# Optimization experiments

Hardware: AMD Instinct MI355X
Metric: run time of the kernel (lower is better)

Reference implementation:

```python
import jax, jax.numpy as jnp
import numpy as np

B, N, HID = 4, 1024, 256
NH, DH = 8, 32          # heads, head dim (HID = NH*DH)
BH = 64                 # bias MLP hidden


def setup_inputs() -> dict:
    key = jax.random.key(0)
    ks = jax.random.split(key, 12)
    s = lambda fan_in: 1.0 / np.sqrt(fan_in)
    return {
        "h": jax.random.normal(ks[0], (B, N, HID), jnp.float32),
        "coord": jax.random.uniform(ks[1], (B, N), jnp.float32),
        "mask": jnp.ones((B, N), jnp.int32),
        # qkv / proj linear params (stored [in, out])
        "Wqkv": jax.random.normal(ks[2], (HID, 3 * HID), jnp.float32) * s(HID),
        "bqkv": jnp.zeros((3 * HID,), jnp.float32),
        "Wproj": jax.random.normal(ks[3], (HID, HID), jnp.float32) * s(HID),
        "bproj": jnp.zeros((HID,), jnp.float32),
        # layernorm
        "gamma": jnp.ones((HID,), jnp.float32),
        "beta": jnp.zeros((HID,), jnp.float32),
        # relative-bias MLP: Linear(1->BH), SiLU, Linear(BH->BH), SiLU, Linear(BH->NH)
        "Wb1": jax.random.normal(ks[4], (1, BH), jnp.float32),
        "bb1": jnp.zeros((BH,), jnp.float32),
        "Wb2": jax.random.normal(ks[5], (BH, BH), jnp.float32) * s(BH),
        "bb2": jnp.zeros((BH,), jnp.float32),
        "Wb3": jax.random.normal(ks[6], (BH, NH), jnp.float32) * s(BH),
        "bb3": jnp.zeros((NH,), jnp.float32),
    }


def _layernorm(x, gamma, beta, eps=1e-5):
    mu = jnp.mean(x, axis=-1, keepdims=True)
    var = jnp.mean((x - mu) ** 2, axis=-1, keepdims=True)
    return (x - mu) * jax.lax.rsqrt(var + eps) * gamma + beta


def reference(h, coord, mask, Wqkv, bqkv, Wproj, bproj, gamma, beta,
              Wb1, bb1, Wb2, bb2, Wb3, bb3):
    x = _layernorm(h, gamma, beta)                      # [B,N,HID]
    qkv = x @ Wqkv + bqkv                               # [B,N,3*HID]
    q, k, v = jnp.split(qkv, 3, axis=-1)
    # [B,N,HID] -> [B,NH,N,DH]
    reshape = lambda t: t.reshape(B, N, NH, DH).transpose(0, 2, 1, 3)
    q, k, v = reshape(q), reshape(k), reshape(v)

    attn = jnp.einsum("bhqd,bhkd->bhqk", q, k) / np.sqrt(DH).astype(np.float32)

    # pairwise coordinate differences and learned bias
    dcoord = coord[:, None, :] - coord[:, :, None]      # [B,N,N]
    t = dcoord[..., None]                               # [B,N,N,1]
    t = jax.nn.silu(t @ Wb1 + bb1)                      # [B,N,N,BH]
    t = jax.nn.silu(t @ Wb2 + bb2)                      # [B,N,N,BH]
    bias = (t @ Wb3 + bb3)                              # [B,N,N,NH]
    attn = attn + bias.transpose(0, 3, 1, 2)            # [B,NH,N,N]

    neg_inf = jnp.array(-jnp.inf, attn.dtype)
    attn = jnp.where(mask[:, None, None, :] == 0, neg_inf, attn)
    w = jax.nn.softmax(attn, axis=-1)

    out = jnp.einsum("bhqk,bhkd->bhqd", w, v)           # [B,NH,N,DH]
    out = out.transpose(0, 2, 1, 3).reshape(B, N, HID)
    out = out @ Wproj + bproj
    return h + out
```

## Files before the change

kernel.cpp:

```cpp
#include <hip/hip_runtime.h>
#include <hip/hip_fp16.h>
#include <math.h>

#define BB   4
#define NN   1024
#define HIDD 256
#define NHD  8
#define DHD  32
#define BHD  64
#define TI4  4096
#define TBS  4104
#define NSPL 2
#define LOG2E 1.4426950408889634f

typedef __attribute__((ext_vector_type(8))) short bf16x8;
typedef __attribute__((ext_vector_type(4))) short bf16x4;
typedef __attribute__((ext_vector_type(4))) float f32x4;

__device__ __forceinline__ unsigned short f2bf(float x) {
  union { float f; unsigned u; } c; c.f = x;
  unsigned r = c.u + 0x7FFFu + ((c.u >> 16) & 1u);
  return (unsigned short)(r >> 16);
}
__device__ __forceinline__ float bf2f(unsigned short b) {
  union { unsigned u; float f; } c; c.u = ((unsigned)b) << 16;
  return c.f;
}

__device__ __forceinline__ void pv_mfma(f32x4& acc, bf16x4 a, bf16x4 b) {
#if __has_builtin(__builtin_amdgcn_mfma_f32_16x16x16bf16_1k)
  acc = __builtin_amdgcn_mfma_f32_16x16x16bf16_1k(a, b, acc, 0, 0, 0);
#else
  asm volatile("s_nop 1\n\t"
               "v_mfma_f32_16x16x16_bf16 %0, %1, %2, %0\n\t"
               "s_nop 7\n\t"
               "s_nop 3"
               : "+v"(acc) : "v"(a), "v"(b));
#endif
}

__global__ __launch_bounds__(256) void prep_kernel(
    const float* __restrict__ Wb1, const float* __restrict__ bb1,
    const float* __restrict__ Wb2, const float* __restrict__ bb2,
    const float* __restrict__ Wb3, const float* __restrict__ bb3,
    const float* __restrict__ Wqkv, const float* __restrict__ Wproj,
    unsigned short* __restrict__ tblb, unsigned short* __restrict__ wtq,
    unsigned short* __restrict__ wtp)
{
  __shared__ float h1a[4][64], h2a[4][64];
  __shared__ float t[16][17];
  int bid = blockIdx.x, tid = threadIdx.x;
  if (bid < 1025) {
    int g = tid >> 6, j = tid & 63;
    int pt = bid * 4 + g;
    float tt = -1.0f + (float)pt * (2.0f / (float)TI4);
    float z0 = fmaf(tt, Wb1[j], bb1[j]);
    h1a[g][j] = z0 / (1.0f + __expf(-z0));
    __syncthreads();
    float a0 = bb2[j];
    #pragma unroll 16
    for (int i = 0; i < BHD; ++i) a0 = fmaf(h1a[g][i], Wb2[i*BHD + j], a0);
    h2a[g][j] = a0 / (1.0f + __expf(-a0));
    __syncthreads();
    if (j < NHD && pt <= TI4) {
      float o0 = bb3[j];
      #pragma unroll 16
      for (int i = 0; i < BHD; ++i) o0 = fmaf(h2a[g][i], Wb3[i*NHD + j], o0);
      tblb[j*TBS + pt] = f2bf(o0 * LOG2E);
    }
  } else {
    const float* W; unsigned short* Wt; int n0, k0, ncols;
    if (bid < 1793) {
      int rb = bid - 1025;
      n0 = (rb % 48) * 16; k0 = (rb / 48) * 16; ncols = 768;
      W = Wqkv; Wt = wtq;
    } else {
      int rc = bid - 1793;
      n0 = (rc & 15) * 16; k0 = (rc >> 4) * 16; ncols = 256;
      W = Wproj; Wt = wtp;
    }
    int sx = tid & 15, sy = tid >> 4;
    t[sy][sx] = W[(size_t)(k0 + sy) * ncols + n0 + sx];
    __syncthreads();
    Wt[(size_t)(n0 + sy) * 256 + k0 + sx] = f2bf(t[sx][sy]);
  }
}

__global__ __launch_bounds__(256) void ln_qkv_mm_kernel(
    const float* __restrict__ h, const float* __restrict__ gamma,
    const float* __restrict__ beta, const unsigned short* __restrict__ Wt,
    const float* __restrict__ bqkv,
    unsigned short* __restrict__ qws, unsigned short* __restrict__ kws,
    unsigned short* __restrict__ vtws)
{
  __shared__ unsigned short xs[16][260];
  int tid = threadIdx.x;
  int m0 = blockIdx.x * 16, n0 = blockIdx.y * 128;

  {
    int r = tid >> 4, q = tid & 15;
    const float* hrow = h + (size_t)(m0 + r)*HIDD + q*16;
    float4 xv[4];
    float sum = 0.f, sq = 0.f;
    #pragma unroll
    for (int j = 0; j < 4; ++j) {
      xv[j] = *(const float4*)&hrow[j*4];
      sum += xv[j].x + xv[j].y + xv[j].z + xv[j].w;
      sq  += xv[j].x*xv[j].x + xv[j].y*xv[j].y + xv[j].z*xv[j].z + xv[j].w*xv[j].w;
    }
    sum += __shfl_xor(sum, 1); sq += __shfl_xor(sq, 1);
    sum += __shfl_xor(sum, 2); sq += __shfl_xor(sq, 2);
    sum += __shfl_xor(sum, 4); sq += __shfl_xor(sq, 4);
    sum += __shfl_xor(sum, 8); sq += __shfl_xor(sq, 8);
    float mu  = sum * (1.0f/HIDD);
    float var = sq  * (1.0f/HIDD) - mu*mu;
    float rs  = rsqrtf(var + 1e-5f);
    #pragma unroll
    for (int j2 = 0; j2 < 2; ++j2) {
      union { bf16x8 v; unsigned short u[8]; } o;
      #pragma unroll
      for (int e = 0; e < 2; ++e) {
        float4 x4 = xv[j2*2 + e];
        int col = q*16 + j2*8 + e*4;
        float4 gv = *(const float4*)&gamma[col];
        float4 bv = *(const float4*)&beta[col];
        o.u[e*4+0] = f2bf(fmaf((x4.x - mu)*rs, gv.x, bv.x));
        o.u[e*4+1] = f2bf(fmaf((x4.y - mu)*rs, gv.y, bv.y));
        o.u[e*4+2] = f2bf(fmaf((x4.z - mu)*rs, gv.z, bv.z));
        o.u[e*4+3] = f2bf(fmaf((x4.w - mu)*rs, gv.w, bv.w));
      }
      *(bf16x8*)&xs[r][q*16 + j2*8] = o.v;
    }
  }
  __syncthreads();

  int lane = tid & 63, w = tid >> 6;
  int lo = lane & 15, hi = lane >> 4;
  int cw = w * 32;
  f32x4 acc[2];
  acc[0] = (f32x4){0.f,0.f,0.f,0.f};
  acc[1] = (f32x4){0.f,0.f,0.f,0.f};

  #pragma unroll
  for (int ks = 0; ks < 8; ++ks) {
    bf16x8 af = *(const bf16x8*)&xs[lo][ks*32 + hi*8];
    #pragma unroll
    for (int nt = 0; nt < 2; ++nt) {
      bf16x8 bf = *(const bf16x8*)&Wt[(size_t)(n0 + cw + nt*16 + lo)*256 + ks*32 + hi*8];
      acc[nt] = __builtin_amdgcn_mfma_f32_16x16x32_bf16(af, bf, acc[nt], 0, 0, 0);
    }
  }

  int b = m0 >> 10;
  if (n0 < 512) {
    unsigned short* dst = (n0 < 256) ? qws : kws;
    int nbase = (m0 & 1023) + hi*4;
    #pragma unroll
    for (int nt = 0; nt < 2; ++nt) {
      int c = n0 + cw + nt*16 + lo;
      int cr = c & 255;
      int head = cr >> 5, d = cr & 31;
      float bq = bqkv[c];
      size_t bh = (size_t)(b*NHD + head);
      #pragma unroll
      for (int r = 0; r < 4; ++r)
        dst[(bh*NN + nbase + r)*DHD + d] = f2bf(acc[nt][r] + bq);
    }
  } else {
    __syncthreads();
    unsigned short (*vt)[20] = (unsigned short(*)[20])&xs[0][0];
    #pragma unroll
    for (int nt = 0; nt < 2; ++nt) {
      int cr = cw + nt*16 + lo;
      float bq = bqkv[n0 + cr];
      union { unsigned short u[4]; unsigned wd[2]; } pk;
      #pragma unroll
      for (int r = 0; r < 4; ++r) pk.u[r] = f2bf(acc[nt][r] + bq);
      int col = hi*4;
      *(unsigned*)&vt[cr][col]     = pk.wd[0];
      *(unsigned*)&vt[cr][col + 2] = pk.wd[1];
    }
    __syncthreads();
    int nn0 = m0 & 1023;
    int row = tid >> 1, ch = tid & 1;
    int cr256 = (n0 - 512) + row;
    int head = cr256 >> 5, d = cr256 & 31;
    *(bf16x8*)&vtws[((size_t)(b*NHD + head)*DHD + d)*NN + nn0 + ch*8] =
        *(const bf16x8*)&vt[row][ch*8];
  }
}

__global__ __launch_bounds__(256, 4) void attn_kernel(
    const unsigned short* __restrict__ Q, const unsigned short* __restrict__ K,
    const unsigned short* __restrict__ Vt, const float* __restrict__ coord,
    const int* __restrict__ mask, const unsigned short* __restrict__ tblb,
    unsigned short* __restrict__ pO, float2* __restrict__ pML)
{
  __shared__ unsigned short tableL[TBS];
  __shared__ unsigned short Klds[2][64][40];
  __shared__ unsigned short Vtlds[2][32][72];
  __shared__ __align__(16) float ckL[NN/NSPL];
  __shared__ __align__(16) int   mkL[NN/NSPL];

  int tid = threadIdx.x, lane = tid & 63, w = tid >> 6;
  int bh = blockIdx.y, half = blockIdx.z;
  int b = bh >> 3, head = bh & 7;
  int qbase = blockIdx.x * 64 + w * 16;
  int lo = lane & 15, hi = lane >> 4;

  {
    const uint4* src = (const uint4*)(tblb + head*TBS);
    uint4* dst = (uint4*)tableL;
    for (int i = tid; i < TBS/8; i += 256) dst[i] = src[i];
  }

  bf16x8 qf = *(const bf16x8*)&Q[((size_t)bh*NN + qbase + lo)*DHD + hi*8];
  float qoff2 = fmaf(coord[b*NN + qbase + lo], -(float)TI4*0.5f, (float)TI4*0.5f);

  float m = -1e30f, l = 0.f;
  f32x4 oacc[2];
  oacc[0] = (f32x4){0.f,0.f,0.f,0.f};
  oacc[1] = (f32x4){0.f,0.f,0.f,0.f};
  const float scale2 = 0.17677669529663689f * LOG2E;

  int kt0 = half * (NN/NSPL);
  int sr = tid >> 2, ss = tid & 3;
  int vr = tid >> 3, vs = tid & 7;
  {
    #pragma unroll
    for (int i = 0; i < (NN/NSPL)/256; ++i) {
      int idx = i*256 + tid;
      ckL[idx] = coord[b*NN + kt0 + idx];
      mkL[idx] = mask [b*NN + kt0 + idx];
    }
    *(bf16x8*)&Klds[0][sr][ss*8] =
        *(const bf16x8*)&K[((size_t)bh*NN + kt0 + sr)*DHD + ss*8];
    *(bf16x8*)&Vtlds[0][vr][vs*8] =
        *(const bf16x8*)&Vt[((size_t)bh*DHD + vr)*NN + kt0 + vs*8];
  }
  __syncthreads();

  for (int t = 0; t < NN/NSPL/64; ++t) {
    int kt = kt0 + t*64;
    int cur = t & 1;
    bf16x8 kn, vn;
    if (t < NN/NSPL/64 - 1) {
      kn = *(const bf16x8*)&K[((size_t)bh*NN + kt + 64 + sr)*DHD + ss*8];
      vn = *(const bf16x8*)&Vt[((size_t)bh*DHD + vr)*NN + kt + 64 + vs*8];
    }
    float ck[4][4]; int mk[4][4];
    #pragma unroll
    for (int nt = 0; nt < 4; ++nt) {
      float4 c4 = *(const float4*)&ckL[t*64 + nt*16 + hi*4];
      int4   m4 = *(const int4*)  &mkL[t*64 + nt*16 + hi*4];
      ck[nt][0] = c4.x; ck[nt][1] = c4.y; ck[nt][2] = c4.z; ck[nt][3] = c4.w;
      mk[nt][0] = m4.x; mk[nt][1] = m4.y; mk[nt][2] = m4.z; mk[nt][3] = m4.w;
    }

    f32x4 z = {0.f,0.f,0.f,0.f};
    f32x4 sacc[4];
    #pragma unroll
    for (int nt = 0; nt < 4; ++nt) {
      bf16x8 kf = *(const bf16x8*)&Klds[cur][nt*16 + lo][hi*8];
      sacc[nt] = __builtin_amdgcn_mfma_f32_16x16x32_bf16(kf, qf, z, 0, 0, 0);
    }

    float sv[4][4];
    #pragma unroll
    for (int nt = 0; nt < 4; ++nt) {
      #pragma unroll
      for (int r = 0; r < 4; ++r) {
        float u = fmaf(ck[nt][r], (float)TI4*0.5f, qoff2);
        int i0 = (int)(u + 0.5f);
        float bias = bf2f(tableL[i0]);
        float s = fmaf(sacc[nt][r], scale2, bias);
        sv[nt][r] = mk[nt][r] ? s : -1e31f;
      }
    }

    float pm = sv[0][0];
    #pragma unroll
    for (int nt = 0; nt < 4; ++nt)
      #pragma unroll
      for (int r = 0; r < 4; ++r) pm = fmaxf(pm, sv[nt][r]);
    pm = fmaxf(pm, __shfl_xor(pm, 16));
    pm = fmaxf(pm, __shfl_xor(pm, 32));
    float mn = fmaxf(m, pm);
    if (mn > m) {
      float sf = __builtin_amdgcn_exp2f(m - mn);
      l *= sf;
      #pragma unroll
      for (int n2 = 0; n2 < 2; ++n2)
        #pragma unroll
        for (int r = 0; r < 4; ++r) oacc[n2][r] *= sf;
      m = mn;
    }

    bf16x4 pfrag[4];
    #pragma unroll
    for (int nt = 0; nt < 4; ++nt) {
      float p0 = __builtin_amdgcn_exp2f(sv[nt][0] - m);
      float p1 = __builtin_amdgcn_exp2f(sv[nt][1] - m);
      float p2 = __builtin_amdgcn_exp2f(sv[nt][2] - m);
      float p3 = __builtin_amdgcn_exp2f(sv[nt][3] - m);
      l += (p0 + p1) + (p2 + p3);
      union { bf16x4 v; unsigned short u[4]; } pk;
      pk.u[0] = f2bf(p0); pk.u[1] = f2bf(p1);
      pk.u[2] = f2bf(p2); pk.u[3] = f2bf(p3);
      pfrag[nt] = pk.v;
    }

    #pragma unroll
    for (int nt = 0; nt < 4; ++nt) {
      #pragma unroll
      for (int n2 = 0; n2 < 2; ++n2) {
        bf16x4 vf = *(const bf16x4*)&Vtlds[cur][n2*16 + lo][nt*16 + hi*4];
        pv_mfma(oacc[n2], vf, pfrag[nt]);
      }
    }

    if (t < NN/NSPL/64 - 1) {
      *(bf16x8*)&Klds[cur^1][sr][ss*8] = kn;
      *(bf16x8*)&Vtlds[cur^1][vr][vs*8] = vn;
    }
    __syncthreads();
  }

  l += __shfl_xor(l, 16);
  l += __shfl_xor(l, 32);
  size_t base = ((size_t)(half*BB*NHD + bh)*NN + qbase + lo);
  #pragma unroll
  for (int n2 = 0; n2 < 2; ++n2) {
    union { bf16x4 v; unsigned short u[4]; } ov;
    ov.u[0] = f2bf(oacc[n2][0]); ov.u[1] = f2bf(oacc[n2][1]);
    ov.u[2] = f2bf(oacc[n2][2]); ov.u[3] = f2bf(oacc[n2][3]);
    *(bf16x4*)&pO[base*DHD + n2*16 + hi*4] = ov.v;
  }
  if (hi == 0) pML[base] = make_float2(m, l);
}

__global__ __launch_bounds__(256) void combine_kernel(
    const unsigned short* __restrict__ pO, const float2* __restrict__ pML,
    unsigned short* __restrict__ aob)
{
  int idx = blockIdx.x * 256 + threadIdx.x;
  int rg = idx >> 2, d8 = (idx & 3) << 3;
  int bh = rg >> 10, n = rg & 1023;
  int b = bh >> 3, head = bh & 7;
  float2 ml0 = pML[rg];
  float2 ml1 = pML[(size_t)(BB*NHD)*NN + rg];
  float mm = fmaxf(ml0.x, ml1.x);
  float e0 = __builtin_amdgcn_exp2f(ml0.x - mm);
  float e1 = __builtin_amdgcn_exp2f(ml1.x - mm);
  float inv = 1.0f / fmaf(ml0.y, e0, ml1.y * e1);
  e0 *= inv; e1 *= inv;
  union { bf16x8 v; unsigned short u[8]; } a, c, o;
  a.v = *(const bf16x8*)&pO[(size_t)rg*DHD + d8];
  c.v = *(const bf16x8*)&pO[((size_t)(BB*NHD)*NN + rg)*DHD + d8];
  #pragma unroll
  for (int e = 0; e < 8; ++e)
    o.u[e] = f2bf(fmaf(bf2f(a.u[e]), e0, bf2f(c.u[e]) * e1));
  *(bf16x8*)&aob[((size_t)(b*NN + n))*HIDD + head*DHD + d8] = o.v;
}

__global__ __launch_bounds__(256) void proj_mm_kernel(
    const unsigned short* __restrict__ AO, const unsigned short* __restrict__ Wpt,
    const float* __restrict__ bp, const float* __restrict__ h,
    float* __restrict__ out)
{
  int tid = threadIdx.x, lane = tid & 63, w = tid >> 6;
  int lo = lane & 15, hi = lane >> 4;
  int m0 = blockIdx.x * 32 + (w & 1) * 16;
  int n0 = blockIdx.y * 32 + (w >> 1) * 16;
  f32x4 acc = (f32x4){0.f,0.f,0.f,0.f};

  #pragma unroll
  for (int ks = 0; ks < 8; ++ks) {
    bf16x8 af = *(const bf16x8*)&AO[(size_t)(m0 + lo)*256 + ks*32 + hi*8];
    bf16x8 bf = *(const bf16x8*)&Wpt[(size_t)(n0 + lo)*256 + ks*32 + hi*8];
    acc = __builtin_amdgcn_mfma_f32_16x16x32_bf16(af, bf, acc, 0, 0, 0);
  }

  int c = n0 + lo;
  float bpv = bp[c];
  #pragma unroll
  for (int r = 0; r < 4; ++r) {
    size_t o = (size_t)(m0 + hi*4 + r)*HIDD + c;
    out[o] = h[o] + acc[r] + bpv;
  }
}

extern "C" void kernel_launch(void* const* d_in, const int* in_sizes, int n_in,
                              void* d_out, int out_size, void* d_ws, size_t ws_size,
                              hipStream_t stream)
{
  const float* h     = (const float*)d_in[0];
  const float* coord = (const float*)d_in[1];
  const int*   mask  = (const int*)  d_in[2];
  const float* Wqkv  = (const float*)d_in[3];
  const float* bqkv  = (const float*)d_in[4];
  const float* Wproj = (const float*)d_in[5];
  const float* bproj = (const float*)d_in[6];
  const float* gamma = (const float*)d_in[7];
  const float* beta  = (const float*)d_in[8];
  const float* Wb1   = (const float*)d_in[9];
  const float* bb1   = (const float*)d_in[10];
  const float* Wb2   = (const float*)d_in[11];
  const float* bb2   = (const float*)d_in[12];
  const float* Wb3   = (const float*)d_in[13];
  const float* bb3   = (const float*)d_in[14];
  float* out = (float*)d_out;

  unsigned short* tblb = (unsigned short*)d_ws;
  float2* pML = (float2*)(tblb + NHD*TBS);
  unsigned short* wtq  = (unsigned short*)(pML + (size_t)NSPL*BB*NHD*NN);
  unsigned short* wtp  = wtq + 768*256;
  unsigned short* qws  = wtp + 256*256;
  unsigned short* kws  = qws + (size_t)BB*NHD*NN*DHD;
  unsigned short* vtws = kws + (size_t)BB*NHD*NN*DHD;
  unsigned short* pO   = vtws + (size_t)BB*NHD*NN*DHD;
  unsigned short* aob  = pO + (size_t)NSPL*BB*NHD*NN*DHD;

  prep_kernel<<<dim3(2049), dim3(256), 0, stream>>>(
      Wb1, bb1, Wb2, bb2, Wb3, bb3, Wqkv, Wproj, tblb, wtq, wtp);
  ln_qkv_mm_kernel<<<dim3(BB*NN/16, 6), dim3(256), 0, stream>>>(
      h, gamma, beta, wtq, bqkv, qws, kws, vtws);
  attn_kernel<<<dim3(NN/64, BB*NHD, NSPL), dim3(256), 0, stream>>>(
      qws, kws, vtws, coord, mask, tblb, pO, pML);
  combine_kernel<<<dim3(512), dim3(256), 0, stream>>>(pO, pML, aob);
  proj_mm_kernel<<<dim3(BB*NN/32, HIDD/32), dim3(256), 0, stream>>>(
      aob, wtp, bproj, h, out);
}
```

Baseline: 65.73 us.

## Fuse split-combine into projection GEMM and use lazy softmax rescaling

Removes the separate combine kernel. The projection kernel now merges the two split-KV partial outputs into shared memory before its MFMA loop, which saves one launch and the aob round trip through global memory. The cost is redundant work: each of the 8 column blocks recomputes the same combine for its 32 rows. The attention inner loop also skips rescaling the running max unless the new max exceeds it by more than 8 (in log2 units), which cuts rescale work but lets exponents grow by up to 2^8 before renormalising.

```diff
diff --git a/kernel.cpp b/kernel.cpp
--- a/kernel.cpp
+++ b/kernel.cpp
@@ -285,8 +285,8 @@
       for (int r = 0; r < 4; ++r) pm = fmaxf(pm, sv[nt][r]);
     pm = fmaxf(pm, __shfl_xor(pm, 16));
     pm = fmaxf(pm, __shfl_xor(pm, 32));
-    float mn = fmaxf(m, pm);
-    if (mn > m) {
+    if (!__all(pm <= m + 8.0f)) {
+      float mn = fmaxf(m, pm);
       float sf = __builtin_amdgcn_exp2f(m - mn);
       l *= sf;
       #pragma unroll
@@ -339,53 +339,58 @@
   if (hi == 0) pML[base] = make_float2(m, l);
 }
 
-__global__ __launch_bounds__(256) void combine_kernel(
+__global__ __launch_bounds__(256) void proj_mm_kernel(
     const unsigned short* __restrict__ pO, const float2* __restrict__ pML,
-    unsigned short* __restrict__ aob)
+    const unsigned short* __restrict__ Wpt, const float* __restrict__ bp,
+    const float* __restrict__ h, float* __restrict__ out)
 {
-  int idx = blockIdx.x * 256 + threadIdx.x;
-  int rg = idx >> 2, d8 = (idx & 3) << 3;
-  int bh = rg >> 10, n = rg & 1023;
-  int b = bh >> 3, head = bh & 7;
-  float2 ml0 = pML[rg];
-  float2 ml1 = pML[(size_t)(BB*NHD)*NN + rg];
-  float mm = fmaxf(ml0.x, ml1.x);
-  float e0 = __builtin_amdgcn_exp2f(ml0.x - mm);
-  float e1 = __builtin_amdgcn_exp2f(ml1.x - mm);
-  float inv = 1.0f / fmaf(ml0.y, e0, ml1.y * e1);
-  e0 *= inv; e1 *= inv;
-  union { bf16x8 v; unsigned short u[8]; } a, c, o;
-  a.v = *(const bf16x8*)&pO[(size_t)rg*DHD + d8];
-  c.v = *(const bf16x8*)&pO[((size_t)(BB*NHD)*NN + rg)*DHD + d8];
-  #pragma unroll
-  for (int e = 0; e < 8; ++e)
-    o.u[e] = f2bf(fmaf(bf2f(a.u[e]), e0, bf2f(c.u[e]) * e1));
-  *(bf16x8*)&aob[((size_t)(b*NN + n))*HIDD + head*DHD + d8] = o.v;
-}
-
-__global__ __launch_bounds__(256) void proj_mm_kernel(
-    const unsigned short* __restrict__ AO, const unsigned short* __restrict__ Wpt,
-    const float* __restrict__ bp, const float* __restrict__ h,
-    float* __restrict__ out)
-{
-  int tid = threadIdx.x, lane = tid & 63, w = tid >> 6;
+  __shared__ unsigned short alds[32][264];
+  int tid = threadIdx.x;
+  int m0 = blockIdx.x * 32, n0 = blockIdx.y * 32;
+
+  {
+    int r = tid >> 3, q = tid & 7;
+    int g = m0 + r, b = g >> 10, n = g & 1023;
+    int bhh = b*NHD + q;
+    float2 ml0 = pML[(size_t)bhh*NN + n];
+    float2 ml1 = pML[((size_t)(BB*NHD) + bhh)*NN + n];
+    float mm = fmaxf(ml0.x, ml1.x);
+    float e0 = __builtin_amdgcn_exp2f(ml0.x - mm);
+    float e1 = __builtin_amdgcn_exp2f(ml1.x - mm);
+    float inv = 1.0f / fmaf(ml0.y, e0, ml1.y * e1);
+    e0 *= inv; e1 *= inv;
+    const bf16x8* p0 = (const bf16x8*)&pO[((size_t)bhh*NN + n)*DHD];
+    const bf16x8* p1 = (const bf16x8*)&pO[(((size_t)(BB*NHD) + bhh)*NN + n)*DHD];
+    #pragma unroll
+    for (int j = 0; j < 4; ++j) {
+      union { bf16x8 v; unsigned short u[8]; } a, c, o;
+      a.v = p0[j]; c.v = p1[j];
+      #pragma unroll
+      for (int e = 0; e < 8; ++e)
+        o.u[e] = f2bf(fmaf(bf2f(a.u[e]), e0, bf2f(c.u[e]) * e1));
+      *(bf16x8*)&alds[r][q*32 + j*8] = o.v;
+    }
+  }
+  __syncthreads();
+
+  int lane = tid & 63, w = tid >> 6;
   int lo = lane & 15, hi = lane >> 4;
-  int m0 = blockIdx.x * 32 + (w & 1) * 16;
-  int n0 = blockIdx.y * 32 + (w >> 1) * 16;
+  int mw = (w & 1) * 16;
+  int nw = n0 + (w >> 1) * 16;
   f32x4 acc = (f32x4){0.f,0.f,0.f,0.f};
 
   #pragma unroll
   for (int ks = 0; ks < 8; ++ks) {
-    bf16x8 af = *(const bf16x8*)&AO[(size_t)(m0 + lo)*256 + ks*32 + hi*8];
-    bf16x8 bf = *(const bf16x8*)&Wpt[(size_t)(n0 + lo)*256 + ks*32 + hi*8];
+    bf16x8 af = *(const bf16x8*)&alds[mw + lo][ks*32 + hi*8];
+    bf16x8 bf = *(const bf16x8*)&Wpt[(size_t)(nw + lo)*256 + ks*32 + hi*8];
     acc = __builtin_amdgcn_mfma_f32_16x16x32_bf16(af, bf, acc, 0, 0, 0);
   }
 
-  int c = n0 + lo;
+  int c = nw + lo;
   float bpv = bp[c];
   #pragma unroll
   for (int r = 0; r < 4; ++r) {
-    size_t o = (size_t)(m0 + hi*4 + r)*HIDD + c;
+    size_t o = (size_t)(m0 + mw + hi*4 + r)*HIDD + c;
     out[o] = h[o] + acc[r] + bpv;
   }
 }
@@ -419,7 +424,6 @@
   unsigned short* kws  = qws + (size_t)BB*NHD*NN*DHD;
   unsigned short* vtws = kws + (size_t)BB*NHD*NN*DHD;
   unsigned short* pO   = vtws + (size_t)BB*NHD*NN*DHD;
-  unsigned short* aob  = pO + (size_t)NSPL*BB*NHD*NN*DHD;
 
   prep_kernel<<<dim3(2049), dim3(256), 0, stream>>>(
       Wb1, bb1, Wb2, bb2, Wb3, bb3, Wqkv, Wproj, tblb, wtq, wtp);
@@ -427,7 +431,6 @@
       h, gamma, beta, wtq, bqkv, qws, kws, vtws);
   attn_kernel<<<dim3(NN/64, BB*NHD, NSPL), dim3(256), 0, stream>>>(
       qws, kws, vtws, coord, mask, tblb, pO, pML);
-  combine_kernel<<<dim3(512), dim3(256), 0, stream>>>(pO, pML, aob);
   proj_mm_kernel<<<dim3(BB*NN/32, HIDD/32), dim3(256), 0, stream>>>(
-      aob, wtp, bproj, h, out);
-}
+      pO, pML, wtp, bproj, h, out);
+}
```

Measured after the change: 64.27 us. -2.2%, faster.
